# Optimization experiments

Hardware: AMD Instinct MI355X
Metric: run time of the kernel (lower is better)

Reference implementation:

```python
import jax, jax.numpy as jnp
import numpy as np

NUM_HEADS = 8

def setup_inputs() -> dict:
    key = jax.random.key(0)
    ks = jax.random.split(key, 5)
    B, N, D = 2, 2048, 512
    x = jax.random.normal(ks[0], (B, N, D), dtype=jnp.float32)
    qkv_w = jax.random.normal(ks[1], (3 * D, D), dtype=jnp.float32) * (D ** -0.5)
    qkv_b = jax.random.normal(ks[2], (3 * D,), dtype=jnp.float32) * 0.02
    proj_w = jax.random.normal(ks[3], (D, D), dtype=jnp.float32) * (D ** -0.5)
    proj_b = jax.random.normal(ks[4], (D,), dtype=jnp.float32) * 0.02
    return {"x": x, "qkv_w": qkv_w, "qkv_b": qkv_b, "proj_w": proj_w, "proj_b": proj_b}

def reference(x, qkv_w, qkv_b, proj_w, proj_b):
    B, N, D = x.shape
    H = NUM_HEADS
    hd = D // H
    scale = hd ** -0.5
    # qkv projection: [B,N,3D] -> [B,N,3,H,hd]
    qkv = (jnp.einsum('bnd,ed->bne', x, qkv_w) + qkv_b).reshape(B, N, 3, H, hd)
    q, k, v = qkv[:, :, 0], qkv[:, :, 1], qkv[:, :, 2]
    q = q * scale
    attn = jnp.einsum('bnhd,bmhd->bhnm', q, k)  # [B,H,N,M]
    # L2-normalize each score row before softmax (the custom modification)
    attn = attn / (jnp.linalg.norm(attn, axis=-1, keepdims=True) + 1e-6)
    attn = jax.nn.softmax(attn, axis=-1)
    out = jnp.einsum('bhnm,bmhd->bnhd', attn, v).reshape(B, N, D)
    return jnp.einsum('bnd,ed->bne', out, proj_w) + proj_b
```

## Files before the change

kernel.cpp:

```cpp
#include <hip/hip_runtime.h>
#include <hip/hip_bf16.h>
#include <cstdint>

typedef __attribute__((ext_vector_type(8))) short short8;
typedef __attribute__((ext_vector_type(4))) float floatx4;

__device__ __forceinline__ float bf2f(unsigned short u) {
  union { unsigned int i; float f; } v;
  v.i = ((unsigned int)u) << 16;
  return v.f;
}
__device__ __forceinline__ unsigned short f2bf(float f) {
  union { float f; unsigned int i; } v; v.f = f;
  unsigned int r = v.i + 0x7FFFu + ((v.i >> 16) & 1u);
  return (unsigned short)(r >> 16);
}

__device__ __forceinline__ void async_copy16(const void* g, void* l) {
  __builtin_amdgcn_global_load_lds(
      (const __attribute__((address_space(1))) void*)g,
      (__attribute__((address_space(3))) void*)l, 16, 0, 0);
}

__global__ __launch_bounds__(256) void convert3_kernel(
    const float* __restrict__ x, const float* __restrict__ w1,
    const float* __restrict__ w2, unsigned short* __restrict__ xb,
    unsigned short* __restrict__ w1b, unsigned short* __restrict__ w2b) {
  constexpr int N0 = 4096 * 512 / 8, N1 = 1536 * 512 / 8, N2 = 512 * 512 / 8;
  int i = blockIdx.x * 256 + threadIdx.x;
  const float* src;
  unsigned short* dst;
  int off;
  if (i < N0) { src = x; dst = xb; off = i; }
  else if (i < N0 + N1) { src = w1; dst = w1b; off = i - N0; }
  else if (i < N0 + N1 + N2) { src = w2; dst = w2b; off = i - N0 - N1; }
  else return;
  const float4* p = (const float4*)src + (size_t)off * 2;
  float4 a = p[0], b = p[1];
  short8 r;
  r[0] = (short)f2bf(a.x); r[1] = (short)f2bf(a.y);
  r[2] = (short)f2bf(a.z); r[3] = (short)f2bf(a.w);
  r[4] = (short)f2bf(b.x); r[5] = (short)f2bf(b.y);
  r[6] = (short)f2bf(b.z); r[7] = (short)f2bf(b.w);
  *(short8*)(dst + (size_t)off * 8) = r;
}

template <int BM, int BN, typename OutT>
__global__ __launch_bounds__(256) void gemm_tiled_kernel(
    const unsigned short* __restrict__ A, const unsigned short* __restrict__ W,
    const float* __restrict__ bias, OutT* __restrict__ out,
    int M, int N, int K) {
  constexpr int BK = 64;
  constexpr int MI = BM / 32;
  constexpr int NI = BN / 32;
  __shared__ __align__(16) unsigned short As[BM * BK];
  __shared__ __align__(16) unsigned short Ws[BN * BK];

  int tid = threadIdx.x, wave = tid >> 6, lane = tid & 63;
  int l16 = lane & 15, quad = lane >> 4;
  int bm = blockIdx.x, bn = blockIdx.y;
  int wm = (wave & 1) * (BM / 2), wn = (wave >> 1) * (BN / 2);

  floatx4 acc[MI][NI] = {};

  for (int kk = 0; kk < K; kk += BK) {
    __syncthreads();
#pragma unroll
    for (int c = 0; c < MI; c++) {
      int ci = (wave * MI + c) * 64 + lane;
      int row = ci >> 3, col8 = (ci & 7) ^ (row & 7);
      async_copy16(A + (size_t)(bm * BM + row) * K + kk + col8 * 8,
                   As + (size_t)ci * 8);
    }
#pragma unroll
    for (int c = 0; c < NI; c++) {
      int ci = (wave * NI + c) * 64 + lane;
      int row = ci >> 3, col8 = (ci & 7) ^ (row & 7);
      async_copy16(W + (size_t)(bn * BN + row) * K + kk + col8 * 8,
                   Ws + (size_t)ci * 8);
    }
    __syncthreads();

#pragma unroll
    for (int k2 = 0; k2 < 2; k2++) {
      short8 a[MI], w8[NI];
#pragma unroll
      for (int mi = 0; mi < MI; mi++) {
        int row = wm + mi * 16 + l16;
        int slot = ((k2 * 4 + quad) ^ (row & 7));
        a[mi] = *(const short8*)(As + row * 64 + slot * 8);
      }
#pragma unroll
      for (int ni = 0; ni < NI; ni++) {
        int row = wn + ni * 16 + l16;
        int slot = ((k2 * 4 + quad) ^ (row & 7));
        w8[ni] = *(const short8*)(Ws + row * 64 + slot * 8);
      }
#pragma unroll
      for (int mi = 0; mi < MI; mi++)
#pragma unroll
        for (int ni = 0; ni < NI; ni++)
          acc[mi][ni] = __builtin_amdgcn_mfma_f32_16x16x32_bf16(
              a[mi], w8[ni], acc[mi][ni], 0, 0, 0);
    }
  }

#pragma unroll
  for (int ni = 0; ni < NI; ni++) {
    int col = bn * BN + wn + ni * 16 + l16;
    float bb = bias[col];
#pragma unroll
    for (int mi = 0; mi < MI; mi++) {
#pragma unroll
      for (int r = 0; r < 4; r++) {
        int row = bm * BM + wm + mi * 16 + quad * 4 + r;
        float v = acc[mi][ni][r] + bb;
        if constexpr (sizeof(OutT) == 2)
          out[(size_t)row * N + col] = (OutT)f2bf(v);
        else
          out[(size_t)row * N + col] = (OutT)v;
      }
    }
  }
}

__global__ __launch_bounds__(256) void kv_transpose_kernel(
    const unsigned short* __restrict__ qkv, unsigned short* __restrict__ kt,
    unsigned short* __restrict__ vt) {
  __shared__ __align__(16) unsigned short TK[64 * 72];
  __shared__ __align__(16) unsigned short TV[64 * 72];
  int nb = blockIdx.x, bh = blockIdx.y;
  int b = bh >> 3, h = bh & 7;
  int t = threadIdx.x;
#pragma unroll
  for (int c = 0; c < 2; c++) {
    int ci = c * 256 + t;
    int row = ci >> 3, ch = ci & 7;
    const unsigned short* src =
        qkv + (size_t)(b * 2048 + nb * 64 + row) * 1536 + h * 64 + ch * 8;
    *(short8*)(TK + row * 72 + ch * 8) = *(const short8*)(src + 512);
    *(short8*)(TV + row * 72 + ch * 8) = *(const short8*)(src + 1024);
  }
  __syncthreads();
  int d = t & 63, nblk = t >> 6;
  short8 k0, k1, v0, v1;
#pragma unroll
  for (int i = 0; i < 8; i++) {
    k0[i] = (short)TK[(nblk * 16 + i) * 72 + d];
    k1[i] = (short)TK[(nblk * 16 + 8 + i) * 72 + d];
    v0[i] = (short)TV[(nblk * 16 + i) * 72 + d];
    v1[i] = (short)TV[(nblk * 16 + 8 + i) * 72 + d];
  }
  size_t orow = ((size_t)bh * 64 + d) * 2048 + nb * 64 + nblk * 16;
  *(short8*)(kt + orow) = k0;
  *(short8*)(kt + orow + 8) = k1;
  *(short8*)(vt + orow) = v0;
  *(short8*)(vt + orow + 8) = v1;
}

__global__ __launch_bounds__(256) void g_partial_kernel(
    const unsigned short* __restrict__ kt, float* __restrict__ gpart) {
  int bh = blockIdx.x, sl = blockIdx.y;
  int tid = threadIdx.x, wave = tid >> 6, lane = tid & 63;
  int l16 = lane & 15, quad = lane >> 4;
  const unsigned short* kb = kt + (size_t)bh * 64 * 2048;

  floatx4 acc[4] = {};
  for (int ks = 0; ks < 16; ks++) {
    int k0 = sl * 512 + ks * 32 + quad * 8;
    short8 a = *(const short8*)(kb + (size_t)(wave * 16 + l16) * 2048 + k0);
#pragma unroll
    for (int dt = 0; dt < 4; dt++) {
      short8 bb = *(const short8*)(kb + (size_t)(dt * 16 + l16) * 2048 + k0);
      acc[dt] = __builtin_amdgcn_mfma_f32_16x16x32_bf16(a, bb, acc[dt], 0, 0, 0);
    }
  }
  float* gout = gpart + ((size_t)(bh * 4 + sl)) * 4096;
#pragma unroll
  for (int dt = 0; dt < 4; dt++)
#pragma unroll
    for (int r = 0; r < 4; r++)
      gout[(wave * 16 + quad * 4 + r) * 64 + dt * 16 + l16] = acc[dt][r];
}

__global__ __launch_bounds__(256) void g_reduce_kernel(
    const float* __restrict__ gpart, unsigned short* __restrict__ gb) {
  int i = blockIdx.x * 256 + threadIdx.x;
  int bh = i >> 12, ed = i & 4095;
  const float* p = gpart + (size_t)(bh * 4) * 4096 + ed;
  gb[i] = f2bf(p[0] + p[4096] + p[8192] + p[12288]);
}

__global__ __launch_bounds__(256) void attn_kernel(
    const unsigned short* __restrict__ qkv,
    const unsigned short* __restrict__ vt,
    const unsigned short* __restrict__ gb,
    unsigned short* __restrict__ attn_out) {
  constexpr int NSEQ = 2048, LD = 1536, DM = 512;
  const float scale = 0.125f;

  __shared__ __align__(16) unsigned short Pb[32 * 128];

  int qb = blockIdx.x, h = blockIdx.y, b = blockIdx.z;
  int tid = threadIdx.x, wave = tid >> 6, lane = tid & 63;
  int l16 = lane & 15, quad = lane >> 4;

  const unsigned short* base = qkv + (size_t)b * NSEQ * LD;
  const unsigned short* vbase = vt + (size_t)(b * 8 + h) * 64 * NSEQ;

  short8 aq[2][2];
#pragma unroll
  for (int mi = 0; mi < 2; mi++) {
    const unsigned short* qp =
        base + (size_t)(qb * 32 + mi * 16 + l16) * LD + h * 64;
    aq[mi][0] = *(const short8*)(qp + quad * 8);
    aq[mi][1] = *(const short8*)(qp + 32 + quad * 8);
  }

  const unsigned short* gbh = gb + (size_t)(b * 8 + h) * 4096;
  float sumsq[2][4] = {};
#pragma unroll
  for (int eti = 0; eti < 4; eti++) {
    floatx4 t[2] = {};
#pragma unroll
    for (int k2 = 0; k2 < 2; k2++) {
      short8 bg = *(const short8*)(gbh + (eti * 16 + l16) * 64 + k2 * 32 + quad * 8);
#pragma unroll
      for (int mi = 0; mi < 2; mi++)
        t[mi] = __builtin_amdgcn_mfma_f32_16x16x32_bf16(aq[mi][k2], bg, t[mi], 0, 0, 0);
    }
#pragma unroll
    for (int mi = 0; mi < 2; mi++)
#pragma unroll
      for (int r = 0; r < 4; r++) {
        float qv = bf2f(base[(size_t)(qb * 32 + mi * 16 + quad * 4 + r) * LD +
                             h * 64 + eti * 16 + l16]);
        sumsq[mi][r] += t[mi][r] * qv;
      }
  }
  float invk[2][4];
#pragma unroll
  for (int mi = 0; mi < 2; mi++)
#pragma unroll
    for (int r = 0; r < 4; r++) {
#pragma unroll
      for (int m = 1; m <= 8; m <<= 1)
        sumsq[mi][r] += __shfl_xor(sumsq[mi][r], m, 64);
      invk[mi][r] = scale / (scale * sqrtf(sumsq[mi][r]) + 1e-6f);
    }

  floatx4 o[2] = {};
  float lsum[2][4] = {};

  for (int mc = 0; mc < NSEQ; mc += 128) {
#pragma unroll
    for (int st = 0; st < 2; st++) {
      int kvrow = mc + wave * 32 + st * 16 + l16;
      const unsigned short* kp = base + (size_t)kvrow * LD + 512 + h * 64;
      floatx4 s[2] = {};
#pragma unroll
      for (int k2 = 0; k2 < 2; k2++) {
        short8 bk = *(const short8*)(kp + k2 * 32 + quad * 8);
#pragma unroll
        for (int mi = 0; mi < 2; mi++)
          s[mi] = __builtin_amdgcn_mfma_f32_16x16x32_bf16(aq[mi][k2], bk, s[mi], 0, 0, 0);
      }
      int kvc = wave * 4 + st * 2 + (l16 >> 3);
#pragma unroll
      for (int mi = 0; mi < 2; mi++)
#pragma unroll
        for (int r = 0; r < 4; r++) {
          float p = __expf(s[mi][r] * invk[mi][r]);
          lsum[mi][r] += p;
          int q = mi * 16 + quad * 4 + r;
          Pb[q * 128 + ((kvc ^ (q & 15)) << 3) + (l16 & 7)] = f2bf(p);
        }
    }
    __syncthreads();

    const unsigned short* vp = vbase + (size_t)(wave * 16 + l16) * NSEQ + mc;
#pragma unroll
    for (int ks = 0; ks < 4; ks++) {
      short8 bv = *(const short8*)(vp + ks * 32 + quad * 8);
#pragma unroll
      for (int mi = 0; mi < 2; mi++) {
        int q = mi * 16 + l16;
        short8 ap = *(const short8*)(Pb + q * 128 + (((ks * 4 + quad) ^ (q & 15)) << 3));
        o[mi] = __builtin_amdgcn_mfma_f32_16x16x32_bf16(ap, bv, o[mi], 0, 0, 0);
      }
    }
    __syncthreads();
  }

#pragma unroll
  for (int mi = 0; mi < 2; mi++)
#pragma unroll
    for (int r = 0; r < 4; r++)
#pragma unroll
      for (int m = 1; m <= 8; m <<= 1)
        lsum[mi][r] += __shfl_xor(lsum[mi][r], m, 64);
  float* Red = (float*)Pb;
  if (l16 == 0) {
#pragma unroll
    for (int mi = 0; mi < 2; mi++)
#pragma unroll
      for (int r = 0; r < 4; r++)
        Red[wave * 32 + mi * 16 + quad * 4 + r] = lsum[mi][r];
  }
  __syncthreads();

  size_t ob = ((size_t)b * NSEQ + qb * 32) * DM + h * 64 + wave * 16 + l16;
#pragma unroll
  for (int mi = 0; mi < 2; mi++)
#pragma unroll
    for (int r = 0; r < 4; r++) {
      int q = mi * 16 + quad * 4 + r;
      float tot = Red[q] + Red[32 + q] + Red[64 + q] + Red[96 + q];
      attn_out[ob + (size_t)q * DM] = f2bf(o[mi][r] / tot);
    }
}

extern "C" void kernel_launch(void* const* d_in, const int* in_sizes, int n_in,
                              void* d_out, int out_size, void* d_ws, size_t ws_size,
                              hipStream_t stream) {
  const float* x = (const float*)d_in[0];
  const float* qkv_w = (const float*)d_in[1];
  const float* qkv_b = (const float*)d_in[2];
  const float* proj_w = (const float*)d_in[3];
  const float* proj_b = (const float*)d_in[4];
  float* out = (float*)d_out;

  unsigned short* xb = (unsigned short*)d_ws;
  unsigned short* qkvw_b = xb + (size_t)4096 * 512;
  unsigned short* projw_b = qkvw_b + (size_t)1536 * 512;
  unsigned short* qkv = projw_b + (size_t)512 * 512;
  unsigned short* attn_out = qkv + (size_t)4096 * 1536;
  unsigned short* vt = attn_out + (size_t)4096 * 512;
  unsigned short* gbuf = vt + (size_t)16 * 64 * 2048;
  unsigned short* kt = xb;
  float* gpart = (float*)qkvw_b;

  convert3_kernel<<<1536, 256, 0, stream>>>(x, qkv_w, proj_w, xb, qkvw_b, projw_b);
  gemm_tiled_kernel<128, 64, unsigned short>
      <<<dim3(4096 / 128, 1536 / 64), 256, 0, stream>>>(
          xb, qkvw_b, qkv_b, qkv, 4096, 1536, 512);
  kv_transpose_kernel<<<dim3(32, 16), 256, 0, stream>>>(qkv, kt, vt);
  g_partial_kernel<<<dim3(16, 4), 256, 0, stream>>>(kt, gpart);
  g_reduce_kernel<<<256, 256, 0, stream>>>(gpart, gbuf);
  attn_kernel<<<dim3(64, 8, 2), 256, 0, stream>>>(qkv, vt, gbuf, attn_out);
  gemm_tiled_kernel<64, 64, float>
      <<<dim3(4096 / 64, 512 / 64), 256, 0, stream>>>(
          attn_out, projw_b, proj_b, out, 4096, 512, 512);
}
```

Baseline: 178.7 us.

## Stage K and V tiles in LDS via async copies; split G reduction further

The attention kernel now copies each 128-row K tile and 64x128 V^T tile into swizzled shared memory with global_load_lds before computing, rather than having each wave load its MFMA operands straight from global memory with strided rows. The G-matrix partial kernel is split into 8 slices instead of 4 for more blocks, with the reduce summing 8 partials and the partial buffer moved to the attn_out region. A launch-bounds occupancy hint of 4 is added. The K/V loads are not double-buffered, so the copies and their synchronisation are exposed on every iteration, and the extra shared memory may limit occupancy.

```diff
diff --git a/kernel.cpp b/kernel.cpp
--- a/kernel.cpp
+++ b/kernel.cpp
@@ -166,8 +166,8 @@
   const unsigned short* kb = kt + (size_t)bh * 64 * 2048;
 
   floatx4 acc[4] = {};
-  for (int ks = 0; ks < 16; ks++) {
-    int k0 = sl * 512 + ks * 32 + quad * 8;
+  for (int ks = 0; ks < 8; ks++) {
+    int k0 = sl * 256 + ks * 32 + quad * 8;
     short8 a = *(const short8*)(kb + (size_t)(wave * 16 + l16) * 2048 + k0);
 #pragma unroll
     for (int dt = 0; dt < 4; dt++) {
@@ -175,7 +175,7 @@
       acc[dt] = __builtin_amdgcn_mfma_f32_16x16x32_bf16(a, bb, acc[dt], 0, 0, 0);
     }
   }
-  float* gout = gpart + ((size_t)(bh * 4 + sl)) * 4096;
+  float* gout = gpart + ((size_t)(bh * 8 + sl)) * 4096;
 #pragma unroll
   for (int dt = 0; dt < 4; dt++)
 #pragma unroll
@@ -187,11 +187,14 @@
     const float* __restrict__ gpart, unsigned short* __restrict__ gb) {
   int i = blockIdx.x * 256 + threadIdx.x;
   int bh = i >> 12, ed = i & 4095;
-  const float* p = gpart + (size_t)(bh * 4) * 4096 + ed;
-  gb[i] = f2bf(p[0] + p[4096] + p[8192] + p[12288]);
-}
-
-__global__ __launch_bounds__(256) void attn_kernel(
+  const float* p = gpart + (size_t)(bh * 8) * 4096 + ed;
+  float s = 0.f;
+#pragma unroll
+  for (int j = 0; j < 8; j++) s += p[j * 4096];
+  gb[i] = f2bf(s);
+}
+
+__global__ __launch_bounds__(256, 4) void attn_kernel(
     const unsigned short* __restrict__ qkv,
     const unsigned short* __restrict__ vt,
     const unsigned short* __restrict__ gb,
@@ -199,6 +202,8 @@
   constexpr int NSEQ = 2048, LD = 1536, DM = 512;
   const float scale = 0.125f;
 
+  __shared__ __align__(16) unsigned short Kb[128 * 64];
+  __shared__ __align__(16) unsigned short Vtb[64 * 128];
   __shared__ __align__(16) unsigned short Pb[32 * 128];
 
   int qb = blockIdx.x, h = blockIdx.y, b = blockIdx.z;
@@ -253,14 +258,31 @@
   float lsum[2][4] = {};
 
   for (int mc = 0; mc < NSEQ; mc += 128) {
+    __syncthreads();
+#pragma unroll
+    for (int c = 0; c < 4; c++) {
+      int ci = (wave * 4 + c) * 64 + lane;
+      int row = ci >> 3, sc = (ci & 7) ^ (row & 7);
+      async_copy16(base + (size_t)(mc + row) * LD + 512 + h * 64 + sc * 8,
+                   Kb + (size_t)ci * 8);
+    }
+#pragma unroll
+    for (int c = 0; c < 4; c++) {
+      int ci = (wave * 4 + c) * 64 + lane;
+      int d = ci >> 4, sc = (ci & 15) ^ (d & 15);
+      async_copy16(vbase + (size_t)d * NSEQ + mc + sc * 8,
+                   Vtb + (size_t)ci * 8);
+    }
+    __syncthreads();
+
 #pragma unroll
     for (int st = 0; st < 2; st++) {
-      int kvrow = mc + wave * 32 + st * 16 + l16;
-      const unsigned short* kp = base + (size_t)kvrow * LD + 512 + h * 64;
+      int row = wave * 32 + st * 16 + l16;
       floatx4 s[2] = {};
 #pragma unroll
       for (int k2 = 0; k2 < 2; k2++) {
-        short8 bk = *(const short8*)(kp + k2 * 32 + quad * 8);
+        short8 bk = *(const short8*)(Kb + row * 64 +
+                                     (((k2 * 4 + quad) ^ (row & 7)) * 8));
 #pragma unroll
         for (int mi = 0; mi < 2; mi++)
           s[mi] = __builtin_amdgcn_mfma_f32_16x16x32_bf16(aq[mi][k2], bk, s[mi], 0, 0, 0);
@@ -278,10 +300,10 @@
     }
     __syncthreads();
 
-    const unsigned short* vp = vbase + (size_t)(wave * 16 + l16) * NSEQ + mc;
+    int d = wave * 16 + l16;
 #pragma unroll
     for (int ks = 0; ks < 4; ks++) {
-      short8 bv = *(const short8*)(vp + ks * 32 + quad * 8);
+      short8 bv = *(const short8*)(Vtb + d * 128 + (((ks * 4 + quad) ^ l16) * 8));
 #pragma unroll
       for (int mi = 0; mi < 2; mi++) {
         int q = mi * 16 + l16;
@@ -289,8 +311,8 @@
         o[mi] = __builtin_amdgcn_mfma_f32_16x16x32_bf16(ap, bv, o[mi], 0, 0, 0);
       }
     }
-    __syncthreads();
-  }
+  }
+  __syncthreads();
 
 #pragma unroll
   for (int mi = 0; mi < 2; mi++)
@@ -338,14 +360,14 @@
   unsigned short* vt = attn_out + (size_t)4096 * 512;
   unsigned short* gbuf = vt + (size_t)16 * 64 * 2048;
   unsigned short* kt = xb;
-  float* gpart = (float*)qkvw_b;
+  float* gpart = (float*)attn_out;
 
   convert3_kernel<<<1536, 256, 0, stream>>>(x, qkv_w, proj_w, xb, qkvw_b, projw_b);
   gemm_tiled_kernel<128, 64, unsigned short>
       <<<dim3(4096 / 128, 1536 / 64), 256, 0, stream>>>(
           xb, qkvw_b, qkv_b, qkv, 4096, 1536, 512);
   kv_transpose_kernel<<<dim3(32, 16), 256, 0, stream>>>(qkv, kt, vt);
-  g_partial_kernel<<<dim3(16, 4), 256, 0, stream>>>(kt, gpart);
+  g_partial_kernel<<<dim3(16, 8), 256, 0, stream>>>(kt, gpart);
   g_reduce_kernel<<<256, 256, 0, stream>>>(gpart, gbuf);
   attn_kernel<<<dim3(64, 8, 2), 256, 0, stream>>>(qkv, vt, gbuf, attn_out);
   gemm_tiled_kernel<64, 64, float>
```

Result: faster. 150.7 us (-15.7%).
